# Kernel tuning notes

Measured on AMD Instinct MI355X. Metric: run time of the kernel, lower is better.

Reference implementation:

```python
import jax, jax.numpy as jnp
import numpy as np

B, T, C, HS = 8, 4096, 1024, 128

def setup_inputs() -> dict:
    key = jax.random.key(0)
    kx, kq, kk, kv = jax.random.split(key, 4)
    x = jax.random.normal(kx, (B, T, C), dtype=jnp.float32)
    # Linear weights stored as [in, out] so projection is x @ W
    Wq = jax.random.normal(kq, (C, HS), dtype=jnp.float32) * (C ** -0.5)
    Wk = jax.random.normal(kk, (C, HS), dtype=jnp.float32) * (C ** -0.5)
    Wv = jax.random.normal(kv, (C, HS), dtype=jnp.float32) * (C ** -0.5)
    return {"x": x, "Wq": Wq, "Wk": Wk, "Wv": Wv}

def reference(x, Wq, Wk, Wv):
    # one head of causal self-attention (dropout=0.0 -> identity)
    q = x @ Wq  # [B,T,HS]
    k = x @ Wk
    v = x @ Wv
    scale = q.shape[-1] ** -0.5
    scores = jnp.einsum('bqd,bkd->bqk', q, k) * scale  # [B,T,T]
    t = q.shape[1]
    causal = jnp.tril(jnp.ones((t, t), dtype=bool))
    scores = jnp.where(causal, scores, jnp.finfo(scores.dtype).min)
    weights = jax.nn.softmax(scores, axis=-1)
    out = jnp.einsum('bqk,bkd->bqd', weights, v)  # [B,T,HS]
    return out
```

## Files before the change

### kernel.cpp

```cpp
#include <hip/hip_runtime.h>
#include <hip/hip_bf16.h>

#define TB 8
#define TT 4096
#define TC 1024
#define THS 128

typedef __bf16 bf16;
typedef __attribute__((ext_vector_type(8))) __bf16 bf16x8;
typedef __attribute__((ext_vector_type(2))) __bf16 bf16x2;
typedef __attribute__((ext_vector_type(4))) float f32x4;
typedef __attribute__((ext_vector_type(16))) float f32x16;

__device__ __forceinline__ unsigned pkbf(float a, float b) {
    bf16x2 t = { (bf16)a, (bf16)b };
    return __builtin_bit_cast(unsigned, t);
}

__device__ __forceinline__ void gload16(const void* g, void* l) {
    __builtin_amdgcn_global_load_lds(
        (const __attribute__((address_space(1))) void*)g,
        (__attribute__((address_space(3))) void*)l, 16, 0, 0);
}

__global__ __launch_bounds__(256) void wt_kernel(const float* __restrict__ Wq,
                                                 const float* __restrict__ Wk,
                                                 const float* __restrict__ Wv,
                                                 bf16* __restrict__ Wt) {
    int idx = blockIdx.x * 256 + threadIdx.x;
    int n = idx & 127;
    int k = (idx >> 7) & 1023;
    int w = idx >> 17;
    const float* W = (w == 0) ? Wq : (w == 1) ? Wk : Wv;
    Wt[((w << 7) + n) * 1024 + k] = (bf16)W[(k << 7) + n];
}

__global__ __launch_bounds__(256, 2) void qkv_kernel(const float* __restrict__ x,
                                                     const bf16* __restrict__ Wt,
                                                     bf16* __restrict__ Q,
                                                     bf16* __restrict__ K,
                                                     bf16* __restrict__ V) {
    __shared__ __align__(1024) char wsm[2][24576];
    __shared__ __align__(1024) char xsm[2][8192];
    const int tid = threadIdx.x;
    const int wave = tid >> 6, lane = tid & 63;
    const int lr = lane & 15, g = lane >> 4;
    const long row0 = (long)blockIdx.x * 64;

    long wOff[6]; int wLoff[6];
    #pragma unroll
    for (int i = 0; i < 6; i++) {
        int D = i * 4096 + wave * 1024 + lane * 16;
        int n = D >> 6, kb2 = D & 63;
        wOff[i] = (long)n * 2048 + (kb2 ^ ((n & 3) << 4));
        wLoff[i] = i * 4096 + wave * 1024;
    }
    long xOff[2]; int xLoff[2];
    #pragma unroll
    for (int i = 0; i < 2; i++) {
        int D = wave * 2048 + i * 1024 + lane * 16;
        int xr = D >> 7, xcb = D & 127;
        xOff[i] = (long)xr * 4096 + (xcb ^ ((xr & 7) << 4));
        xLoff[i] = wave * 2048 + i * 1024;
    }
    const char* xb = (const char*)x + row0 * 4096;
    const char* wb = (const char*)Wt;

    f32x4 acc[4][6] = {};

    {
        #pragma unroll
        for (int i = 0; i < 6; i++) gload16(wb + wOff[i], &wsm[0][0] + wLoff[i]);
        #pragma unroll
        for (int i = 0; i < 2; i++) gload16(xb + xOff[i], &xsm[0][0] + xLoff[i]);
    }
    asm volatile("s_waitcnt vmcnt(0)" ::: "memory");
    __builtin_amdgcn_s_barrier();

    const int asw = (lr & 7) << 4;
    const int bsw = (lr & 3) << 4;
    #pragma unroll 1
    for (int s = 0; s < 32; s++) {
        const int bi = s & 1;
        if (s + 1 < 32) {
            const char* wsrc = wb + (long)(s + 1) * 64;
            const char* xsrc = xb + (long)(s + 1) * 128;
            #pragma unroll
            for (int i = 0; i < 6; i++) gload16(wsrc + wOff[i], &wsm[bi ^ 1][0] + wLoff[i]);
            #pragma unroll
            for (int i = 0; i < 2; i++) gload16(xsrc + xOff[i], &xsm[bi ^ 1][0] + xLoff[i]);
        }
        const char* xp = &xsm[bi][0];
        const char* wp = &wsm[bi][0];
        bf16x8 a[4];
        #pragma unroll
        for (int ar = 0; ar < 4; ar++) {
            const int rbase = (ar * 16 + lr) * 128;
            f32x4 lo = *reinterpret_cast<const f32x4*>(xp + rbase + ((g * 32) ^ asw));
            f32x4 hi4 = *reinterpret_cast<const f32x4*>(xp + rbase + ((g * 32 + 16) ^ asw));
            uint4 u;
            u.x = pkbf(lo[0], lo[1]); u.y = pkbf(lo[2], lo[3]);
            u.z = pkbf(hi4[0], hi4[1]); u.w = pkbf(hi4[2], hi4[3]);
            a[ar] = __builtin_bit_cast(bf16x8, u);
        }
        #pragma unroll
        for (int nt = 0; nt < 6; nt++) {
            const int n = wave * 96 + nt * 16 + lr;
            bf16x8 bfr = *reinterpret_cast<const bf16x8*>(wp + n * 64 + ((g * 16) ^ bsw));
            #pragma unroll
            for (int ar = 0; ar < 4; ar++)
                acc[ar][nt] = __builtin_amdgcn_mfma_f32_16x16x32_bf16(a[ar], bfr, acc[ar][nt], 0, 0, 0);
        }
        asm volatile("s_waitcnt vmcnt(0)" ::: "memory");
        __builtin_amdgcn_s_barrier();
    }
    const float qscale = 0.08838834764831845f;
    bf16* outs[3] = {Q, K, V};
    #pragma unroll
    for (int nt = 0; nt < 6; nt++) {
        const int col = wave * 96 + nt * 16 + lr;
        const int w = col >> 7, d = col & 127;
        #pragma unroll
        for (int ar = 0; ar < 4; ar++)
            #pragma unroll
            for (int r = 0; r < 4; r++) {
                float val = acc[ar][nt][r];
                if (w == 0) val *= qscale;
                long row = row0 + ar * 16 + g * 4 + r;
                outs[w][row * 128 + d] = (bf16)val;
            }
    }
}

__global__ __launch_bounds__(256) void vtrans_kernel(const bf16* __restrict__ V,
                                                     bf16* __restrict__ Vt) {
    __shared__ __align__(16) bf16 tile[64][136];
    const int tid = threadIdx.x;
    const int b = blockIdx.y;
    const int t0 = blockIdx.x * 64;
    const long ibase = ((long)b * TT + t0) * 128;
    #pragma unroll
    for (int i = 0; i < 4; i++) {
        int slot = tid + 256 * i;
        int r = slot >> 4, c8 = (slot & 15) * 8;
        *reinterpret_cast<bf16x8*>(&tile[r][c8]) =
            *reinterpret_cast<const bf16x8*>(&V[ibase + r * 128 + c8]);
    }
    __syncthreads();
    #pragma unroll
    for (int i = 0; i < 4; i++) {
        int slot = tid + 256 * i;
        int d = slot >> 3, t8 = (slot & 7) * 8;
        bf16x8 v;
        #pragma unroll
        for (int j = 0; j < 8; j++) v[j] = tile[t8 + j][d];
        *reinterpret_cast<bf16x8*>(&Vt[((long)b * 128 + d) * TT + t0 + t8]) = v;
    }
}

__global__ __launch_bounds__(512, 2) void attn_kernel(const bf16* __restrict__ Q,
                                                      const bf16* __restrict__ K,
                                                      const bf16* __restrict__ Vt,
                                                      float* __restrict__ out) {
    __shared__ __align__(1024) char smem[131072];
    const int tid = threadIdx.x;
    const int wave = tid >> 6, lane = tid & 63;
    const int c = lane & 31, hi = lane >> 5;
    const int qs = wave & 1, qq = wave >> 1;
    const int ksw = (c & 7) << 4, vsw = (c & 3) << 4;
    const int v = blockIdx.x >> 3, b = blockIdx.x & 7;
    const long base = (long)b * TT * 128;
    const char* Kb = (const char*)(K + base);
    const char* Vb = (const char*)(Vt + (long)b * 128 * TT);
    char* kB[2] = { smem + qq * 16384, smem + qq * 16384 + 8192 };
    char* vB[2] = { smem + 65536 + qq * 16384, smem + 65536 + qq * 16384 + 8192 };
    float* mm = (float*)(smem + 98304);
    float* ll = (float*)(smem + 99072);

    long kOff[4], vOff[4]; int lOff[4];
    #pragma unroll
    for (int i = 0; i < 4; i++) {
        int D = qs * 4096 + i * 1024 + lane * 16;
        int kr = D >> 8, kcb = D & 255;
        kOff[i] = kr * 256 + (kcb ^ ((kr & 7) << 4));
        int vr = D >> 6, vcb = D & 63;
        vOff[i] = (long)vr * 8192 + (vcb ^ ((vr & 3) << 4));
        lOff[i] = qs * 4096 + i * 1024;
    }

    #pragma unroll 1
    for (int ph = 0; ph < 2; ph++) {
        const int qt = ph ? 63 - v : v;
        const int ntile = 2 * (qt + 1);
        const int nIt = (ntile + 3) >> 2;
        const int q0w = qt * 64 + qs * 32;
        const int qa = q0w + c;

        bf16x8 qf[8];
        #pragma unroll
        for (int dw = 0; dw < 8; dw++)
            qf[dw] = *reinterpret_cast<const bf16x8*>(&Q[base + (long)qa * 128 + dw * 16 + hi * 8]);

        f32x16 O[4] = {};
        float m = -__builtin_inff(), l = 0.f;

        if (qq < ntile) {
            const char* Ks = Kb + (long)qq * 8192;
            const char* Vs = Vb + (long)qq * 64;
            #pragma unroll
            for (int i = 0; i < 4; i++) {
                gload16(Ks + kOff[i], kB[0] + lOff[i]);
                gload16(Vs + vOff[i], vB[0] + lOff[i]);
            }
        }
        asm volatile("s_waitcnt vmcnt(0)" ::: "memory");
        __builtin_amdgcn_s_barrier();

        #pragma unroll 1
        for (int it = 0; it < nIt; it++) {
            const int bi = it & 1;
            const int t = qq + 4 * it;
            const int tn = t + 4;
            if (tn < ntile) {
                const char* Ks = Kb + (long)tn * 8192;
                const char* Vs = Vb + (long)tn * 64;
                #pragma unroll
                for (int i = 0; i < 4; i++) {
                    gload16(Ks + kOff[i], kB[bi ^ 1] + lOff[i]);
                    gload16(Vs + vOff[i], vB[bi ^ 1] + lOff[i]);
                }
            }
            const int kv0 = t * 32;
            if (t < ntile && kv0 <= q0w + 31) {
                const char* kb = kB[bi];
                const char* vb = vB[bi];
                f32x16 S = {};
                #pragma unroll
                for (int dw = 0; dw < 8; dw++) {
                    bf16x8 kf = *reinterpret_cast<const bf16x8*>(
                        kb + c * 256 + ((dw * 32 + hi * 16) ^ ksw));
                    S = __builtin_amdgcn_mfma_f32_32x32x16_bf16(kf, qf[dw], S, 0, 0, 0);
                }
                if (kv0 + 31 > q0w) {
                    #pragma unroll
                    for (int i = 0; i < 16; i++) {
                        int kvr = kv0 + (i & 3) + 8 * (i >> 2) + 4 * hi;
                        if (kvr > qa) S[i] = -__builtin_inff();
                    }
                }
                float t8[8];
                #pragma unroll
                for (int i = 0; i < 8; i++) t8[i] = fmaxf(S[i], S[i + 8]);
                float t4a = fmaxf(t8[0], t8[4]), t4b = fmaxf(t8[1], t8[5]);
                float t4c = fmaxf(t8[2], t8[6]), t4d = fmaxf(t8[3], t8[7]);
                float pm = fmaxf(fmaxf(t4a, t4b), fmaxf(t4c, t4d));
                pm = fmaxf(pm, __shfl_xor(pm, 32, 64));
                if (!__all(pm - m <= 8.0f)) {
                    float mn = fmaxf(m, pm);
                    float fr = __expf(m - mn);
                    #pragma unroll
                    for (int dt = 0; dt < 4; dt++) O[dt] = O[dt] * fr;
                    l *= fr;
                    m = mn;
                }
                #pragma unroll
                for (int i = 0; i < 16; i++) S[i] = __expf(S[i] - m);
                float s8[8];
                #pragma unroll
                for (int i = 0; i < 8; i++) s8[i] = S[i] + S[i + 8];
                l += ((s8[0] + s8[4]) + (s8[1] + s8[5])) + ((s8[2] + s8[6]) + (s8[3] + s8[7]));

                bf16x8 pf[2];
                #pragma unroll
                for (int wl = 0; wl < 2; wl++) {
                    const int i0 = 8 * wl;
                    unsigned L0 = pkbf(S[i0 + 0], S[i0 + 1]);
                    unsigned L1 = pkbf(S[i0 + 2], S[i0 + 3]);
                    unsigned H0 = pkbf(S[i0 + 4], S[i0 + 5]);
                    unsigned H1 = pkbf(S[i0 + 6], S[i0 + 7]);
                    unsigned XL0 = __shfl_xor((int)L0, 32, 64);
                    unsigned XL1 = __shfl_xor((int)L1, 32, 64);
                    unsigned XH0 = __shfl_xor((int)H0, 32, 64);
                    unsigned XH1 = __shfl_xor((int)H1, 32, 64);
                    uint4 f;
                    f.x = hi ? XH0 : L0;
                    f.y = hi ? XH1 : L1;
                    f.z = hi ? H0 : XL0;
                    f.w = hi ? H1 : XL1;
                    pf[wl] = __builtin_bit_cast(bf16x8, f);
                }
                #pragma unroll
                for (int wl = 0; wl < 2; wl++)
                    #pragma unroll
                    for (int dt = 0; dt < 4; dt++) {
                        bf16x8 vf = *reinterpret_cast<const bf16x8*>(
                            vb + (dt * 32 + c) * 64 + ((wl * 32 + hi * 16) ^ vsw));
                        O[dt] = __builtin_amdgcn_mfma_f32_32x32x16_bf16(vf, pf[wl], O[dt], 0, 0, 0);
                    }
            }
            asm volatile("s_waitcnt vmcnt(0)" ::: "memory");
            __builtin_amdgcn_s_barrier();
        }

        l += __shfl_xor(l, 32, 64);

        if (qq != 0) {
            const int sl = (qq - 1) * 2 + qs;
            char* om = smem + sl * 16384;
            #pragma unroll
            for (int dt = 0; dt < 4; dt++)
                #pragma unroll
                for (int g = 0; g < 4; g++) {
                    float4 w4 = { O[dt][4 * g + 0], O[dt][4 * g + 1],
                                  O[dt][4 * g + 2], O[dt][4 * g + 3] };
                    *reinterpret_cast<float4*>(
                        om + c * 512 + ((dt * 128 + g * 32 + hi * 16) ^ ((c & 7) << 4))) = w4;
                }
            if (hi == 0) { mm[sl * 32 + c] = m; ll[sl * 32 + c] = l; }
        }
        __syncthreads();
        if (qq == 0) {
            float mq[3], lq[3];
            float mx = m;
            #pragma unroll
            for (int p = 0; p < 3; p++) {
                const int sl = p * 2 + qs;
                mq[p] = mm[sl * 32 + c];
                lq[p] = ll[sl * 32 + c];
                mx = fmaxf(mx, mq[p]);
            }
            float f0 = __expf(m - mx);
            float lt = l * f0;
            float fq[3];
            #pragma unroll
            for (int p = 0; p < 3; p++) { fq[p] = __expf(mq[p] - mx); lt += lq[p] * fq[p]; }
            float linv = 1.0f / lt;
            #pragma unroll
            for (int dt = 0; dt < 4; dt++)
                #pragma unroll
                for (int g = 0; g < 4; g++) {
                    float4 r;
                    r.x = O[dt][4 * g + 0] * f0;
                    r.y = O[dt][4 * g + 1] * f0;
                    r.z = O[dt][4 * g + 2] * f0;
                    r.w = O[dt][4 * g + 3] * f0;
                    #pragma unroll
                    for (int p = 0; p < 3; p++) {
                        const char* om = smem + (p * 2 + qs) * 16384;
                        float4 o1 = *reinterpret_cast<const float4*>(
                            om + c * 512 + ((dt * 128 + g * 32 + hi * 16) ^ ((c & 7) << 4)));
                        r.x += o1.x * fq[p]; r.y += o1.y * fq[p];
                        r.z += o1.z * fq[p]; r.w += o1.w * fq[p];
                    }
                    r.x *= linv; r.y *= linv; r.z *= linv; r.w *= linv;
                    *reinterpret_cast<float4*>(
                        &out[base + (long)qa * 128 + dt * 32 + 8 * g + 4 * hi]) = r;
                }
        }
        __syncthreads();
    }
}

extern "C" void kernel_launch(void* const* d_in, const int* in_sizes, int n_in,
                              void* d_out, int out_size, void* d_ws, size_t ws_size,
                              hipStream_t stream) {
    const float* x  = (const float*)d_in[0];
    const float* Wq = (const float*)d_in[1];
    const float* Wk = (const float*)d_in[2];
    const float* Wv = (const float*)d_in[3];
    float* out = (float*)d_out;
    bf16* Q  = (bf16*)d_ws;
    bf16* K  = Q  + (size_t)32768 * 128;
    bf16* V  = K  + (size_t)32768 * 128;
    bf16* Wt = V  + (size_t)32768 * 128;
    bf16* Vt = Wt + (size_t)3 * 128 * 1024;
    wt_kernel<<<1536, 256, 0, stream>>>(Wq, Wk, Wv, Wt);
    qkv_kernel<<<512, 256, 0, stream>>>(x, Wt, Q, K, V);
    vtrans_kernel<<<dim3(64, 8), 256, 0, stream>>>(V, Vt);
    attn_kernel<<<256, 512, 0, stream>>>(Q, K, Vt, out);
}
```

Measured before the change: 137.8 us.

## Restructure attention to 128-row query tiles with 64-wide KV blocks and two-way split

The attention kernel now has each block handle a 128-row query tile, with four query sub-tiles of 32 rows. The KV range is split across only two waves per sub-tile, each processing 64-key blocks, so there are two score MFMAs per step. V is stored in tile-blocked layout (64 tokens by 128 dims) with new swizzles, and the final merge combines two partials instead of four. This is meant to halve per-iteration barrier and softmax overhead and reduce the merge work. The weight-transpose kernel is also rewritten to use a shared-memory tile for coalesced access. The trade-off is more registers per wave and coarser causal load balancing.

Result: slower. 181.0 us (+31.4%).

```diff
diff --git a/kernel.cpp b/kernel.cpp
--- a/kernel.cpp
+++ b/kernel.cpp
@@ -27,12 +27,29 @@
                                                  const float* __restrict__ Wk,
                                                  const float* __restrict__ Wv,
                                                  bf16* __restrict__ Wt) {
-    int idx = blockIdx.x * 256 + threadIdx.x;
-    int n = idx & 127;
-    int k = (idx >> 7) & 1023;
-    int w = idx >> 17;
+    __shared__ float tile[64][65];
+    const int tid = threadIdx.x;
+    const int idx = blockIdx.x;
+    const int w = idx >> 5;
+    const int kt = (idx & 31) >> 1, ntb = idx & 1;
+    const int k0 = kt * 64, n0 = ntb * 64;
     const float* W = (w == 0) ? Wq : (w == 1) ? Wk : Wv;
-    Wt[((w << 7) + n) * 1024 + k] = (bf16)W[(k << 7) + n];
+    #pragma unroll
+    for (int i = 0; i < 4; i++) {
+        int r = (tid >> 4) + i * 16;
+        int c4 = (tid & 15) * 4;
+        float4 x4 = *reinterpret_cast<const float4*>(&W[(long)(k0 + r) * 128 + n0 + c4]);
+        tile[r][c4 + 0] = x4.x; tile[r][c4 + 1] = x4.y;
+        tile[r][c4 + 2] = x4.z; tile[r][c4 + 3] = x4.w;
+    }
+    __syncthreads();
+    const int n = tid >> 2, kk = (tid & 3) * 16;
+    bf16 o[16];
+    #pragma unroll
+    for (int j = 0; j < 16; j++) o[j] = (bf16)tile[kk + j][n];
+    bf16* dst = &Wt[(long)((w << 7) + n0 + n) * 1024 + k0 + kk];
+    *reinterpret_cast<bf16x8*>(dst)     = *reinterpret_cast<bf16x8*>(&o[0]);
+    *reinterpret_cast<bf16x8*>(dst + 8) = *reinterpret_cast<bf16x8*>(&o[8]);
 }
 
 __global__ __launch_bounds__(256, 2) void qkv_kernel(const float* __restrict__ x,
@@ -133,12 +150,12 @@
 }
 
 __global__ __launch_bounds__(256) void vtrans_kernel(const bf16* __restrict__ V,
-                                                     bf16* __restrict__ Vt) {
+                                                     bf16* __restrict__ Vtt) {
     __shared__ __align__(16) bf16 tile[64][136];
     const int tid = threadIdx.x;
     const int b = blockIdx.y;
-    const int t0 = blockIdx.x * 64;
-    const long ibase = ((long)b * TT + t0) * 128;
+    const int tt = blockIdx.x;
+    const long ibase = ((long)b * TT + tt * 64) * 128;
     #pragma unroll
     for (int i = 0; i < 4; i++) {
         int slot = tid + 256 * i;
@@ -154,46 +171,46 @@
         bf16x8 v;
         #pragma unroll
         for (int j = 0; j < 8; j++) v[j] = tile[t8 + j][d];
-        *reinterpret_cast<bf16x8*>(&Vt[((long)b * 128 + d) * TT + t0 + t8]) = v;
+        *reinterpret_cast<bf16x8*>(&Vtt[(((long)b * 64 + tt) * 128 + d) * 64 + t8]) = v;
     }
 }
 
 __global__ __launch_bounds__(512, 2) void attn_kernel(const bf16* __restrict__ Q,
                                                       const bf16* __restrict__ K,
-                                                      const bf16* __restrict__ Vt,
+                                                      const bf16* __restrict__ Vtt,
                                                       float* __restrict__ out) {
     __shared__ __align__(1024) char smem[131072];
     const int tid = threadIdx.x;
     const int wave = tid >> 6, lane = tid & 63;
     const int c = lane & 31, hi = lane >> 5;
-    const int qs = wave & 1, qq = wave >> 1;
-    const int ksw = (c & 7) << 4, vsw = (c & 3) << 4;
+    const int qs = wave >> 1, h = wave & 1;
+    const int kswz = ((c & 7) << 4) ^ (((c >> 3) & 1) << 7);
+    const int vswz = (c & 7) << 4;
     const int v = blockIdx.x >> 3, b = blockIdx.x & 7;
     const long base = (long)b * TT * 128;
     const char* Kb = (const char*)(K + base);
-    const char* Vb = (const char*)(Vt + (long)b * 128 * TT);
-    char* kB[2] = { smem + qq * 16384, smem + qq * 16384 + 8192 };
-    char* vB[2] = { smem + 65536 + qq * 16384, smem + 65536 + qq * 16384 + 8192 };
-    float* mm = (float*)(smem + 98304);
-    float* ll = (float*)(smem + 99072);
+    const char* Vb = (const char*)Vtt + (long)b * 64 * 16384;
+    char* kB[2] = { smem + h * 32768, smem + h * 32768 + 16384 };
+    char* vB[2] = { smem + 65536 + h * 32768, smem + 65536 + h * 32768 + 16384 };
+    float* ml = (float*)(smem + 65536);
 
     long kOff[4], vOff[4]; int lOff[4];
     #pragma unroll
     for (int i = 0; i < 4; i++) {
         int D = qs * 4096 + i * 1024 + lane * 16;
         int kr = D >> 8, kcb = D & 255;
-        kOff[i] = kr * 256 + (kcb ^ ((kr & 7) << 4));
-        int vr = D >> 6, vcb = D & 63;
-        vOff[i] = (long)vr * 8192 + (vcb ^ ((vr & 3) << 4));
+        kOff[i] = kr * 256 + (kcb ^ (((kr & 7) << 4) ^ (((kr >> 3) & 1) << 7)));
+        int vr = D >> 7, vcb = D & 127;
+        vOff[i] = vr * 128 + (vcb ^ ((vr & 7) << 4));
         lOff[i] = qs * 4096 + i * 1024;
     }
 
     #pragma unroll 1
     for (int ph = 0; ph < 2; ph++) {
-        const int qt = ph ? 63 - v : v;
-        const int ntile = 2 * (qt + 1);
-        const int nIt = (ntile + 3) >> 2;
-        const int q0w = qt * 64 + qs * 32;
+        const int qt = ph ? 31 - v : v;
+        const int ntile = 2 * qt + 2;
+        const int nIt = qt + 1;
+        const int q0w = qt * 128 + qs * 32;
         const int qa = q0w + c;
 
         bf16x8 qf[8];
@@ -204,9 +221,9 @@
         f32x16 O[4] = {};
         float m = -__builtin_inff(), l = 0.f;
 
-        if (qq < ntile) {
-            const char* Ks = Kb + (long)qq * 8192;
-            const char* Vs = Vb + (long)qq * 64;
+        {
+            const char* Ks = Kb + (long)h * 16384;
+            const char* Vs = Vb + (long)h * 16384;
             #pragma unroll
             for (int i = 0; i < 4; i++) {
                 gload16(Ks + kOff[i], kB[0] + lOff[i]);
@@ -219,38 +236,42 @@
         #pragma unroll 1
         for (int it = 0; it < nIt; it++) {
             const int bi = it & 1;
-            const int t = qq + 4 * it;
-            const int tn = t + 4;
-            if (tn < ntile) {
-                const char* Ks = Kb + (long)tn * 8192;
-                const char* Vs = Vb + (long)tn * 64;
+            const int t = h + 2 * it;
+            if (t + 2 < ntile) {
+                const char* Ks = Kb + (long)(t + 2) * 16384;
+                const char* Vs = Vb + (long)(t + 2) * 16384;
                 #pragma unroll
                 for (int i = 0; i < 4; i++) {
                     gload16(Ks + kOff[i], kB[bi ^ 1] + lOff[i]);
                     gload16(Vs + vOff[i], vB[bi ^ 1] + lOff[i]);
                 }
             }
-            const int kv0 = t * 32;
-            if (t < ntile && kv0 <= q0w + 31) {
+            const int kv0 = t * 64;
+            if (kv0 <= q0w + 31) {
                 const char* kb = kB[bi];
                 const char* vb = vB[bi];
-                f32x16 S = {};
+                f32x16 S0 = {}, S1 = {};
                 #pragma unroll
                 for (int dw = 0; dw < 8; dw++) {
-                    bf16x8 kf = *reinterpret_cast<const bf16x8*>(
-                        kb + c * 256 + ((dw * 32 + hi * 16) ^ ksw));
-                    S = __builtin_amdgcn_mfma_f32_32x32x16_bf16(kf, qf[dw], S, 0, 0, 0);
-                }
-                if (kv0 + 31 > q0w) {
+                    bf16x8 k0 = *reinterpret_cast<const bf16x8*>(
+                        kb + c * 256 + ((dw * 32 + hi * 16) ^ kswz));
+                    S0 = __builtin_amdgcn_mfma_f32_32x32x16_bf16(k0, qf[dw], S0, 0, 0, 0);
+                    bf16x8 k1 = *reinterpret_cast<const bf16x8*>(
+                        kb + 8192 + c * 256 + ((dw * 32 + hi * 16) ^ kswz));
+                    S1 = __builtin_amdgcn_mfma_f32_32x32x16_bf16(k1, qf[dw], S1, 0, 0, 0);
+                }
+                if (kv0 + 63 > q0w) {
                     #pragma unroll
                     for (int i = 0; i < 16; i++) {
                         int kvr = kv0 + (i & 3) + 8 * (i >> 2) + 4 * hi;
-                        if (kvr > qa) S[i] = -__builtin_inff();
+                        if (kvr > qa)      S0[i] = -__builtin_inff();
+                        if (kvr + 32 > qa) S1[i] = -__builtin_inff();
                     }
                 }
                 float t8[8];
                 #pragma unroll
-                for (int i = 0; i < 8; i++) t8[i] = fmaxf(S[i], S[i + 8]);
+                for (int i = 0; i < 8; i++)
+                    t8[i] = fmaxf(fmaxf(S0[i], S0[i + 8]), fmaxf(S1[i], S1[i + 8]));
                 float t4a = fmaxf(t8[0], t8[4]), t4b = fmaxf(t8[1], t8[5]);
                 float t4c = fmaxf(t8[2], t8[6]), t4d = fmaxf(t8[3], t8[7]);
                 float pm = fmaxf(fmaxf(t4a, t4b), fmaxf(t4c, t4d));
@@ -264,38 +285,49 @@
                     m = mn;
                 }
                 #pragma unroll
-                for (int i = 0; i < 16; i++) S[i] = __expf(S[i] - m);
+                for (int i = 0; i < 16; i++) {
+                    S0[i] = __expf(S0[i] - m);
+                    S1[i] = __expf(S1[i] - m);
+                }
                 float s8[8];
                 #pragma unroll
-                for (int i = 0; i < 8; i++) s8[i] = S[i] + S[i + 8];
+                for (int i = 0; i < 8; i++)
+                    s8[i] = (S0[i] + S0[i + 8]) + (S1[i] + S1[i + 8]);
                 l += ((s8[0] + s8[4]) + (s8[1] + s8[5])) + ((s8[2] + s8[6]) + (s8[3] + s8[7]));
 
-                bf16x8 pf[2];
-                #pragma unroll
-                for (int wl = 0; wl < 2; wl++) {
-                    const int i0 = 8 * wl;
-                    unsigned L0 = pkbf(S[i0 + 0], S[i0 + 1]);
-                    unsigned L1 = pkbf(S[i0 + 2], S[i0 + 3]);
-                    unsigned H0 = pkbf(S[i0 + 4], S[i0 + 5]);
-                    unsigned H1 = pkbf(S[i0 + 6], S[i0 + 7]);
-                    unsigned XL0 = __shfl_xor((int)L0, 32, 64);
-                    unsigned XL1 = __shfl_xor((int)L1, 32, 64);
-                    unsigned XH0 = __shfl_xor((int)H0, 32, 64);
-                    unsigned XH1 = __shfl_xor((int)H1, 32, 64);
-                    uint4 f;
-                    f.x = hi ? XH0 : L0;
-                    f.y = hi ? XH1 : L1;
-                    f.z = hi ? H0 : XL0;
-                    f.w = hi ? H1 : XL1;
-                    pf[wl] = __builtin_bit_cast(bf16x8, f);
-                }
-                #pragma unroll
-                for (int wl = 0; wl < 2; wl++)
+                bf16x8 pf[4];
+                #pragma unroll
+                for (int st = 0; st < 2; st++) {
+                    #pragma unroll
+                    for (int wl = 0; wl < 2; wl++) {
+                        const int i0 = 8 * wl;
+                        unsigned L0, L1, H0, H1;
+                        if (st == 0) {
+                            L0 = pkbf(S0[i0 + 0], S0[i0 + 1]); L1 = pkbf(S0[i0 + 2], S0[i0 + 3]);
+                            H0 = pkbf(S0[i0 + 4], S0[i0 + 5]); H1 = pkbf(S0[i0 + 6], S0[i0 + 7]);
+                        } else {
+                            L0 = pkbf(S1[i0 + 0], S1[i0 + 1]); L1 = pkbf(S1[i0 + 2], S1[i0 + 3]);
+                            H0 = pkbf(S1[i0 + 4], S1[i0 + 5]); H1 = pkbf(S1[i0 + 6], S1[i0 + 7]);
+                        }
+                        unsigned XL0 = __shfl_xor((int)L0, 32, 64);
+                        unsigned XL1 = __shfl_xor((int)L1, 32, 64);
+                        unsigned XH0 = __shfl_xor((int)H0, 32, 64);
+                        unsigned XH1 = __shfl_xor((int)H1, 32, 64);
+                        uint4 f;
+                        f.x = hi ? XH0 : L0;
+                        f.y = hi ? XH1 : L1;
+                        f.z = hi ? H0  : XL0;
+                        f.w = hi ? H1  : XL1;
+                        pf[st * 2 + wl] = __builtin_bit_cast(bf16x8, f);
+                    }
+                }
+                #pragma unroll
+                for (int w4 = 0; w4 < 4; w4++)
                     #pragma unroll
                     for (int dt = 0; dt < 4; dt++) {
                         bf16x8 vf = *reinterpret_cast<const bf16x8*>(
-                            vb + (dt * 32 + c) * 64 + ((wl * 32 + hi * 16) ^ vsw));
-                        O[dt] = __builtin_amdgcn_mfma_f32_32x32x16_bf16(vf, pf[wl], O[dt], 0, 0, 0);
+                            vb + (dt * 32 + c) * 128 + ((w4 * 32 + hi * 16) ^ vswz));
+                        O[dt] = __builtin_amdgcn_mfma_f32_32x32x16_bf16(vf, pf[w4], O[dt], 0, 0, 0);
                     }
             }
             asm volatile("s_waitcnt vmcnt(0)" ::: "memory");
@@ -304,55 +336,37 @@
 
         l += __shfl_xor(l, 32, 64);
 
-        if (qq != 0) {
-            const int sl = (qq - 1) * 2 + qs;
-            char* om = smem + sl * 16384;
+        if (h == 1) {
+            char* om = smem + qs * 16384;
             #pragma unroll
             for (int dt = 0; dt < 4; dt++)
                 #pragma unroll
                 for (int g = 0; g < 4; g++) {
-                    float4 w4 = { O[dt][4 * g + 0], O[dt][4 * g + 1],
-                                  O[dt][4 * g + 2], O[dt][4 * g + 3] };
+                    float4 w4v = { O[dt][4 * g + 0], O[dt][4 * g + 1],
+                                   O[dt][4 * g + 2], O[dt][4 * g + 3] };
                     *reinterpret_cast<float4*>(
-                        om + c * 512 + ((dt * 128 + g * 32 + hi * 16) ^ ((c & 7) << 4))) = w4;
-                }
-            if (hi == 0) { mm[sl * 32 + c] = m; ll[sl * 32 + c] = l; }
+                        om + c * 512 + ((dt * 128 + g * 32 + hi * 16) ^ ((c & 7) << 4))) = w4v;
+                }
+            if (hi == 0) { ml[qs * 64 + c] = m; ml[qs * 64 + 32 + c] = l; }
         }
         __syncthreads();
-        if (qq == 0) {
-            float mq[3], lq[3];
-            float mx = m;
-            #pragma unroll
-            for (int p = 0; p < 3; p++) {
-                const int sl = p * 2 + qs;
-                mq[p] = mm[sl * 32 + c];
-                lq[p] = ll[sl * 32 + c];
-                mx = fmaxf(mx, mq[p]);
-            }
-            float f0 = __expf(m - mx);
-            float lt = l * f0;
-            float fq[3];
-            #pragma unroll
-            for (int p = 0; p < 3; p++) { fq[p] = __expf(mq[p] - mx); lt += lq[p] * fq[p]; }
-            float linv = 1.0f / lt;
+        if (h == 0) {
+            float m1 = ml[qs * 64 + c], l1 = ml[qs * 64 + 32 + c];
+            float mx = fmaxf(m, m1);
+            float f0 = __expf(m - mx), f1 = __expf(m1 - mx);
+            float linv = 1.0f / (l * f0 + l1 * f1);
+            const char* om = smem + qs * 16384;
             #pragma unroll
             for (int dt = 0; dt < 4; dt++)
                 #pragma unroll
                 for (int g = 0; g < 4; g++) {
+                    float4 o1 = *reinterpret_cast<const float4*>(
+                        om + c * 512 + ((dt * 128 + g * 32 + hi * 16) ^ ((c & 7) << 4)));
                     float4 r;
-                    r.x = O[dt][4 * g + 0] * f0;
-                    r.y = O[dt][4 * g + 1] * f0;
-                    r.z = O[dt][4 * g + 2] * f0;
-                    r.w = O[dt][4 * g + 3] * f0;
-                    #pragma unroll
-                    for (int p = 0; p < 3; p++) {
-                        const char* om = smem + (p * 2 + qs) * 16384;
-                        float4 o1 = *reinterpret_cast<const float4*>(
-                            om + c * 512 + ((dt * 128 + g * 32 + hi * 16) ^ ((c & 7) << 4)));
-                        r.x += o1.x * fq[p]; r.y += o1.y * fq[p];
-                        r.z += o1.z * fq[p]; r.w += o1.w * fq[p];
-                    }
-                    r.x *= linv; r.y *= linv; r.z *= linv; r.w *= linv;
+                    r.x = (O[dt][4 * g + 0] * f0 + o1.x * f1) * linv;
+                    r.y = (O[dt][4 * g + 1] * f0 + o1.y * f1) * linv;
+                    r.z = (O[dt][4 * g + 2] * f0 + o1.z * f1) * linv;
+                    r.w = (O[dt][4 * g + 3] * f0 + o1.w * f1) * linv;
                     *reinterpret_cast<float4*>(
                         &out[base + (long)qa * 128 + dt * 32 + 8 * g + 4 * hi]) = r;
                 }
@@ -369,13 +383,13 @@
     const float* Wk = (const float*)d_in[2];
     const float* Wv = (const float*)d_in[3];
     float* out = (float*)d_out;
-    bf16* Q  = (bf16*)d_ws;
-    bf16* K  = Q  + (size_t)32768 * 128;
-    bf16* V  = K  + (size_t)32768 * 128;
-    bf16* Wt = V  + (size_t)32768 * 128;
-    bf16* Vt = Wt + (size_t)3 * 128 * 1024;
-    wt_kernel<<<1536, 256, 0, stream>>>(Wq, Wk, Wv, Wt);
+    bf16* Q   = (bf16*)d_ws;
+    bf16* K   = Q   + (size_t)32768 * 128;
+    bf16* V   = K   + (size_t)32768 * 128;
+    bf16* Wt  = V   + (size_t)32768 * 128;
+    bf16* Vtt = Wt  + (size_t)3 * 128 * 1024;
+    wt_kernel<<<96, 256, 0, stream>>>(Wq, Wk, Wv, Wt);
     qkv_kernel<<<512, 256, 0, stream>>>(x, Wt, Q, K, V);
-    vtrans_kernel<<<dim3(64, 8), 256, 0, stream>>>(V, Vt);
-    attn_kernel<<<256, 512, 0, stream>>>(Q, K, Vt, out);
-}
+    vtrans_kernel<<<dim3(64, 8), 256, 0, stream>>>(V, Vtt);
+    attn_kernel<<<256, 512, 0, stream>>>(Q, K, Vtt, out);
+}
```

## Restructure attention KV pipeline with shared 128-row tiles and tiled V layout

Applied to the files above, without the earlier changes.

The attention kernel now has all 8 waves cooperatively load a shared 128-row K/V tile, double-buffered with prefetch two iterations ahead and a partial vmcnt wait, replacing the per-wave-pair private buffers. V is stored in a tiled 64-token-block layout so each tile is one contiguous chunk, and the swizzles are changed to match. The change also adds s_setprio around the MFMA sections, trims the P-fragment shuffle from four shuffles to two, and rewrites the weight transpose as an LDS-tiled kernel with coalesced accesses. The aim is fewer redundant global loads and better overlap of load latency with compute, at the cost of more complex barrier and wait-count logic.

Measured after the change: 116.9 us. 1.18x faster.

```diff
diff --git a/kernel.cpp b/kernel.cpp
--- a/kernel.cpp
+++ b/kernel.cpp
@@ -27,12 +27,29 @@
                                                  const float* __restrict__ Wk,
                                                  const float* __restrict__ Wv,
                                                  bf16* __restrict__ Wt) {
-    int idx = blockIdx.x * 256 + threadIdx.x;
-    int n = idx & 127;
-    int k = (idx >> 7) & 1023;
-    int w = idx >> 17;
+    __shared__ float tile[64][65];
+    const int tid = threadIdx.x;
+    const int idx = blockIdx.x;
+    const int w = idx >> 5;
+    const int kt = (idx & 31) >> 1, ntb = idx & 1;
+    const int k0 = kt * 64, n0 = ntb * 64;
     const float* W = (w == 0) ? Wq : (w == 1) ? Wk : Wv;
-    Wt[((w << 7) + n) * 1024 + k] = (bf16)W[(k << 7) + n];
+    #pragma unroll
+    for (int i = 0; i < 4; i++) {
+        int r = (tid >> 4) + i * 16;
+        int c4 = (tid & 15) * 4;
+        float4 x4 = *reinterpret_cast<const float4*>(&W[(long)(k0 + r) * 128 + n0 + c4]);
+        tile[r][c4 + 0] = x4.x; tile[r][c4 + 1] = x4.y;
+        tile[r][c4 + 2] = x4.z; tile[r][c4 + 3] = x4.w;
+    }
+    __syncthreads();
+    const int n = tid >> 2, kk = (tid & 3) * 16;
+    bf16 o[16];
+    #pragma unroll
+    for (int j = 0; j < 16; j++) o[j] = (bf16)tile[kk + j][n];
+    bf16* dst = &Wt[(long)((w << 7) + n0 + n) * 1024 + k0 + kk];
+    *reinterpret_cast<bf16x8*>(dst)     = *reinterpret_cast<bf16x8*>(&o[0]);
+    *reinterpret_cast<bf16x8*>(dst + 8) = *reinterpret_cast<bf16x8*>(&o[8]);
 }
 
 __global__ __launch_bounds__(256, 2) void qkv_kernel(const float* __restrict__ x,
@@ -133,12 +150,12 @@
 }
 
 __global__ __launch_bounds__(256) void vtrans_kernel(const bf16* __restrict__ V,
-                                                     bf16* __restrict__ Vt) {
+                                                     bf16* __restrict__ Vtt) {
     __shared__ __align__(16) bf16 tile[64][136];
     const int tid = threadIdx.x;
     const int b = blockIdx.y;
-    const int t0 = blockIdx.x * 64;
-    const long ibase = ((long)b * TT + t0) * 128;
+    const int tt = blockIdx.x;
+    const long ibase = ((long)b * TT + tt * 64) * 128;
     #pragma unroll
     for (int i = 0; i < 4; i++) {
         int slot = tid + 256 * i;
@@ -154,45 +171,40 @@
         bf16x8 v;
         #pragma unroll
         for (int j = 0; j < 8; j++) v[j] = tile[t8 + j][d];
-        *reinterpret_cast<bf16x8*>(&Vt[((long)b * 128 + d) * TT + t0 + t8]) = v;
+        *reinterpret_cast<bf16x8*>(&Vtt[(((long)b * 64 + tt) * 128 + d) * 64 + t8]) = v;
     }
 }
 
 __global__ __launch_bounds__(512, 2) void attn_kernel(const bf16* __restrict__ Q,
                                                       const bf16* __restrict__ K,
-                                                      const bf16* __restrict__ Vt,
+                                                      const bf16* __restrict__ Vtt,
                                                       float* __restrict__ out) {
     __shared__ __align__(1024) char smem[131072];
+    __shared__ float mlb[6 * 64];
     const int tid = threadIdx.x;
     const int wave = tid >> 6, lane = tid & 63;
     const int c = lane & 31, hi = lane >> 5;
-    const int qs = wave & 1, qq = wave >> 1;
-    const int ksw = (c & 7) << 4, vsw = (c & 3) << 4;
+    const int qs = wave >> 2, kvq = wave & 3;
+    const int kswz = ((c & 7) << 4) ^ (((c >> 3) & 1) << 7);
+    const int vswz = (c & 7) << 4;
     const int v = blockIdx.x >> 3, b = blockIdx.x & 7;
     const long base = (long)b * TT * 128;
     const char* Kb = (const char*)(K + base);
-    const char* Vb = (const char*)(Vt + (long)b * 128 * TT);
-    char* kB[2] = { smem + qq * 16384, smem + qq * 16384 + 8192 };
-    char* vB[2] = { smem + 65536 + qq * 16384, smem + 65536 + qq * 16384 + 8192 };
-    float* mm = (float*)(smem + 98304);
-    float* ll = (float*)(smem + 99072);
-
-    long kOff[4], vOff[4]; int lOff[4];
+    const char* Vb = (const char*)Vtt + (long)b * (64 * 16384);
+
+    int kOff[4], vOff[4], lOff[4];
     #pragma unroll
     for (int i = 0; i < 4; i++) {
-        int D = qs * 4096 + i * 1024 + lane * 16;
-        int kr = D >> 8, kcb = D & 255;
-        kOff[i] = kr * 256 + (kcb ^ ((kr & 7) << 4));
-        int vr = D >> 6, vcb = D & 63;
-        vOff[i] = (long)vr * 8192 + (vcb ^ ((vr & 3) << 4));
-        lOff[i] = qs * 4096 + i * 1024;
+        int D = wave * 4096 + i * 1024 + lane * 16;
+        kOff[i] = (D & ~255) | ((D & 255) ^ (((D >> 8) & 7) << 4) ^ (((D >> 11) & 1) << 7));
+        vOff[i] = (D & ~127) | ((D & 127) ^ (((D >> 7) & 7) << 4));
+        lOff[i] = wave * 4096 + i * 1024;
     }
 
     #pragma unroll 1
     for (int ph = 0; ph < 2; ph++) {
         const int qt = ph ? 63 - v : v;
-        const int ntile = 2 * (qt + 1);
-        const int nIt = (ntile + 3) >> 2;
+        const int nIt = (qt + 2) >> 1;
         const int q0w = qt * 64 + qs * 32;
         const int qa = q0w + c;
 
@@ -204,44 +216,45 @@
         f32x16 O[4] = {};
         float m = -__builtin_inff(), l = 0.f;
 
-        if (qq < ntile) {
-            const char* Ks = Kb + (long)qq * 8192;
-            const char* Vs = Vb + (long)qq * 64;
+        {
             #pragma unroll
             for (int i = 0; i < 4; i++) {
-                gload16(Ks + kOff[i], kB[0] + lOff[i]);
-                gload16(Vs + vOff[i], vB[0] + lOff[i]);
-            }
-        }
-        asm volatile("s_waitcnt vmcnt(0)" ::: "memory");
-        __builtin_amdgcn_s_barrier();
+                gload16(Kb + kOff[i], smem + lOff[i]);
+                gload16(Vb + vOff[i], smem + 65536 + lOff[i]);
+            }
+            if (nIt > 1) {
+                #pragma unroll
+                for (int i = 0; i < 4; i++) {
+                    gload16(Kb + 32768 + kOff[i], smem + 32768 + lOff[i]);
+                    gload16(Vb + 32768 + vOff[i], smem + 98304 + lOff[i]);
+                }
+            }
+        }
 
         #pragma unroll 1
         for (int it = 0; it < nIt; it++) {
             const int bi = it & 1;
-            const int t = qq + 4 * it;
-            const int tn = t + 4;
-            if (tn < ntile) {
-                const char* Ks = Kb + (long)tn * 8192;
-                const char* Vs = Vb + (long)tn * 64;
-                #pragma unroll
-                for (int i = 0; i < 4; i++) {
-                    gload16(Ks + kOff[i], kB[bi ^ 1] + lOff[i]);
-                    gload16(Vs + vOff[i], vB[bi ^ 1] + lOff[i]);
-                }
-            }
-            const int kv0 = t * 32;
-            if (t < ntile && kv0 <= q0w + 31) {
-                const char* kb = kB[bi];
-                const char* vb = vB[bi];
+            char* kBuf = smem + bi * 32768;
+            char* vBuf = smem + 65536 + bi * 32768;
+            if (it + 1 < nIt) asm volatile("s_waitcnt vmcnt(8)" ::: "memory");
+            else              asm volatile("s_waitcnt vmcnt(0)" ::: "memory");
+            __builtin_amdgcn_s_barrier();
+
+            const int kv0 = it * 128 + kvq * 32;
+            if (kv0 <= q0w) {
+                const char* kb = kBuf + kvq * 8192;
+                const char* vb = vBuf + (kvq >> 1) * 16384;
+                const int vcol0 = (kvq & 1) * 64;
                 f32x16 S = {};
+                __builtin_amdgcn_s_setprio(1);
                 #pragma unroll
                 for (int dw = 0; dw < 8; dw++) {
                     bf16x8 kf = *reinterpret_cast<const bf16x8*>(
-                        kb + c * 256 + ((dw * 32 + hi * 16) ^ ksw));
+                        kb + c * 256 + ((dw * 32 + hi * 16) ^ kswz));
                     S = __builtin_amdgcn_mfma_f32_32x32x16_bf16(kf, qf[dw], S, 0, 0, 0);
                 }
-                if (kv0 + 31 > q0w) {
+                __builtin_amdgcn_s_setprio(0);
+                if (kv0 == q0w) {
                     #pragma unroll
                     for (int i = 0; i < 16; i++) {
                         int kvr = kv0 + (i & 3) + 8 * (i >> 2) + 4 * hi;
@@ -278,34 +291,44 @@
                     unsigned L1 = pkbf(S[i0 + 2], S[i0 + 3]);
                     unsigned H0 = pkbf(S[i0 + 4], S[i0 + 5]);
                     unsigned H1 = pkbf(S[i0 + 6], S[i0 + 7]);
-                    unsigned XL0 = __shfl_xor((int)L0, 32, 64);
-                    unsigned XL1 = __shfl_xor((int)L1, 32, 64);
-                    unsigned XH0 = __shfl_xor((int)H0, 32, 64);
-                    unsigned XH1 = __shfl_xor((int)H1, 32, 64);
+                    unsigned sel0 = hi ? L0 : H0;
+                    unsigned sel1 = hi ? L1 : H1;
+                    unsigned x0 = __shfl_xor((int)sel0, 32, 64);
+                    unsigned x1 = __shfl_xor((int)sel1, 32, 64);
                     uint4 f;
-                    f.x = hi ? XH0 : L0;
-                    f.y = hi ? XH1 : L1;
-                    f.z = hi ? H0 : XL0;
-                    f.w = hi ? H1 : XL1;
+                    f.x = hi ? x0 : L0;
+                    f.y = hi ? x1 : L1;
+                    f.z = hi ? H0 : x0;
+                    f.w = hi ? H1 : x1;
                     pf[wl] = __builtin_bit_cast(bf16x8, f);
                 }
+                __builtin_amdgcn_s_setprio(1);
                 #pragma unroll
                 for (int wl = 0; wl < 2; wl++)
                     #pragma unroll
                     for (int dt = 0; dt < 4; dt++) {
                         bf16x8 vf = *reinterpret_cast<const bf16x8*>(
-                            vb + (dt * 32 + c) * 64 + ((wl * 32 + hi * 16) ^ vsw));
+                            vb + (dt * 32 + c) * 128 + ((vcol0 + wl * 32 + hi * 16) ^ vswz));
                         O[dt] = __builtin_amdgcn_mfma_f32_32x32x16_bf16(vf, pf[wl], O[dt], 0, 0, 0);
                     }
-            }
-            asm volatile("s_waitcnt vmcnt(0)" ::: "memory");
+                __builtin_amdgcn_s_setprio(0);
+            }
             __builtin_amdgcn_s_barrier();
+            if (it + 2 < nIt) {
+                const char* Ks = Kb + (long)(it + 2) * 32768;
+                const char* Vs = Vb + (long)(it + 2) * 32768;
+                #pragma unroll
+                for (int i = 0; i < 4; i++) {
+                    gload16(Ks + kOff[i], kBuf + lOff[i]);
+                    gload16(Vs + vOff[i], vBuf + lOff[i]);
+                }
+            }
         }
 
         l += __shfl_xor(l, 32, 64);
 
-        if (qq != 0) {
-            const int sl = (qq - 1) * 2 + qs;
+        if (kvq != 0) {
+            const int sl = qs * 3 + (kvq - 1);
             char* om = smem + sl * 16384;
             #pragma unroll
             for (int dt = 0; dt < 4; dt++)
@@ -316,17 +339,17 @@
                     *reinterpret_cast<float4*>(
                         om + c * 512 + ((dt * 128 + g * 32 + hi * 16) ^ ((c & 7) << 4))) = w4;
                 }
-            if (hi == 0) { mm[sl * 32 + c] = m; ll[sl * 32 + c] = l; }
+            if (hi == 0) { mlb[sl * 64 + c] = m; mlb[sl * 64 + 32 + c] = l; }
         }
         __syncthreads();
-        if (qq == 0) {
+        if (kvq == 0) {
             float mq[3], lq[3];
             float mx = m;
             #pragma unroll
             for (int p = 0; p < 3; p++) {
-                const int sl = p * 2 + qs;
-                mq[p] = mm[sl * 32 + c];
-                lq[p] = ll[sl * 32 + c];
+                const int sl = qs * 3 + p;
+                mq[p] = mlb[sl * 64 + c];
+                lq[p] = mlb[sl * 64 + 32 + c];
                 mx = fmaxf(mx, mq[p]);
             }
             float f0 = __expf(m - mx);
@@ -346,7 +369,7 @@
                     r.w = O[dt][4 * g + 3] * f0;
                     #pragma unroll
                     for (int p = 0; p < 3; p++) {
-                        const char* om = smem + (p * 2 + qs) * 16384;
+                        const char* om = smem + (qs * 3 + p) * 16384;
                         float4 o1 = *reinterpret_cast<const float4*>(
                             om + c * 512 + ((dt * 128 + g * 32 + hi * 16) ^ ((c & 7) << 4)));
                         r.x += o1.x * fq[p]; r.y += o1.y * fq[p];
@@ -369,13 +392,13 @@
     const float* Wk = (const float*)d_in[2];
     const float* Wv = (const float*)d_in[3];
     float* out = (float*)d_out;
-    bf16* Q  = (bf16*)d_ws;
-    bf16* K  = Q  + (size_t)32768 * 128;
-    bf16* V  = K  + (size_t)32768 * 128;
-    bf16* Wt = V  + (size_t)32768 * 128;
-    bf16* Vt = Wt + (size_t)3 * 128 * 1024;
-    wt_kernel<<<1536, 256, 0, stream>>>(Wq, Wk, Wv, Wt);
+    bf16* Q   = (bf16*)d_ws;
+    bf16* K   = Q   + (size_t)32768 * 128;
+    bf16* V   = K   + (size_t)32768 * 128;
+    bf16* Wt  = V   + (size_t)32768 * 128;
+    bf16* Vtt = Wt  + (size_t)3 * 128 * 1024;
+    wt_kernel<<<96, 256, 0, stream>>>(Wq, Wk, Wv, Wt);
     qkv_kernel<<<512, 256, 0, stream>>>(x, Wt, Q, K, V);
-    vtrans_kernel<<<dim3(64, 8), 256, 0, stream>>>(V, Vt);
-    attn_kernel<<<256, 512, 0, stream>>>(Q, K, Vt, out);
-}
+    vtrans_kernel<<<dim3(64, 8), 256, 0, stream>>>(V, Vtt);
+    attn_kernel<<<256, 512, 0, stream>>>(Q, K, Vtt, out);
+}
```
